# Performance work log

Hardware: AMD Instinct MI355X
Metric: run time of the kernel (lower is better)

Reference implementation:

```python
import jax, jax.numpy as jnp
import numpy as np

COST_CLS, COST_MASK, COST_DICE = 2.0, 5.0, 5.0


def setup_inputs() -> dict:
    key = jax.random.key(0)
    k1, k2, k3, k4 = jax.random.split(key, 4)
    B, Q, C, H, W, T, Hg, Wg = 4, 100, 81, 256, 256, 20, 512, 512
    pred_logits = jax.random.normal(k1, (B, Q, C), dtype=jnp.float32)
    pred_masks = jax.random.normal(k2, (B, Q, H, W), dtype=jnp.float32)
    # binary GT instance masks (original uses 0/1 masks)
    tgt_masks = (jax.random.uniform(k3, (B, T, Hg, Wg)) < 0.5).astype(jnp.float32)
    tgt_labels = jax.random.randint(k4, (B, T), 0, C).astype(jnp.int64)
    return {"pred_logits": pred_logits, "pred_masks": pred_masks,
            "tgt_masks": tgt_masks, "tgt_labels": tgt_labels}


def _cost_matrices(pred_logits, pred_masks, tgt_masks, tgt_labels):
    # pred_logits [B,Q,C], pred_masks [B,Q,H,W], tgt_masks [B,T,Hg,Wg], tgt_labels [B,T]
    B, Q, H, W = pred_masks.shape
    T, Hg, Wg = tgt_masks.shape[1:]
    # F.interpolate(mode='nearest') down to pred mask size: src = floor(dst * in/out)
    ri = (jnp.arange(H) * Hg) // H
    ci = (jnp.arange(W) * Wg) // W
    tgt = tgt_masks[:, :, ri][:, :, :, ci]          # [B,T,H,W]
    pm = pred_masks.reshape(B, Q, H * W)            # [B,Q,HW]
    tm = tgt.reshape(B, T, H * W)                   # [B,T,HW]
    hw = float(H * W)
    # classification cost: -softmax(logits)[:, tgt_ids]
    prob = jax.nn.softmax(pred_logits, axis=-1)     # [B,Q,C]
    cost_class = -jnp.take_along_axis(prob, tgt_labels[:, None, :], axis=2)  # [B,Q,T]
    # batch_sigmoid_ce_loss: mean over pixels of BCE-with-logits vs 0/1 target
    pos = jax.nn.softplus(-pm)                      # -log sigmoid(x)
    neg = jax.nn.softplus(pm)                       # -log (1 - sigmoid(x))
    cost_mask = (jnp.einsum('bqp,btp->bqt', pos, tm)
                 + jnp.einsum('bqp,btp->bqt', neg, 1.0 - tm)) / hw
    # batch_dice_loss
    sig = jax.nn.sigmoid(pm)
    numer = 2.0 * jnp.einsum('bqp,btp->bqt', sig, tm)
    denom = sig.sum(-1)[:, :, None] + tm.sum(-1)[:, None, :]
    cost_dice = 1.0 - (numer + 1.0) / (denom + 1.0)
    C = COST_CLS * cost_class + COST_MASK * cost_mask + COST_DICE * cost_dice
    return jnp.nan_to_num(C, nan=0.0)               # [B,Q,T]


_cost_jit = jax.jit(_cost_matrices)


def _lsa(cost):
    """Shortest-augmenting-path linear sum assignment (scipy algorithm).
    cost: (R, Cn) numpy array with R <= Cn. Returns col4row[r] = assigned column."""
    R, Cn = cost.shape
    u = np.zeros(R, dtype=np.float64)
    v = np.zeros(Cn, dtype=np.float64)
    col4row = np.full(R, -1, dtype=np.int64)
    row4col = np.full(Cn, -1, dtype=np.int64)
    cost = cost.astype(np.float64)
    for cur_row in range(R):
        shortest = np.full(Cn, np.inf)
        path = np.full(Cn, -1, dtype=np.int64)
        SR = np.zeros(R, dtype=bool)
        SC = np.zeros(Cn, dtype=bool)
        i = cur_row
        minVal = 0.0
        sink = -1
        while sink == -1:
            SR[i] = True
            rem = np.where(~SC)[0]
            d = minVal + cost[i, rem] - u[i] - v[rem]
            upd = d < shortest[rem]
            shortest[rem[upd]] = d[upd]
            path[rem[upd]] = i
            jloc = rem[np.argmin(shortest[rem])]
            minVal = shortest[jloc]
            SC[jloc] = True
            if row4col[jloc] == -1:
                sink = jloc
            else:
                i = row4col[jloc]
        u[cur_row] += minVal
        mask = SR.copy(); mask[cur_row] = False
        u[mask] += minVal - shortest[col4row[mask]]
        v[SC] -= minVal - shortest[SC]
        j = sink
        while True:
            i = path[j]
            row4col[j] = i
            col4row[i], j = j, col4row[i]
            if i == cur_row:
                break
    return col4row


def reference(pred_logits, pred_masks, tgt_masks, tgt_labels):
    C = _cost_jit(pred_logits, pred_masks, tgt_masks, tgt_labels)  # [B,Q,T]
    Cn = np.asarray(C)
    B, Q, T = Cn.shape
    pred_idx, tgt_idx = [], []
    for b in range(B):
        # solve on the transpose (T <= Q): target t -> query q[t]
        q = _lsa(Cn[b].T)
        t = np.arange(T)
        order = np.argsort(q)  # scipy returns row (query) indices in sorted order
        pred_idx.append(q[order])
        tgt_idx.append(t[order])
    return (C,
            jnp.asarray(np.stack(pred_idx), dtype=jnp.int64),
            jnp.asarray(np.stack(tgt_idx), dtype=jnp.int64))
```

## Files before the change

kernel.cpp:

```cpp
#include <hip/hip_runtime.h>
#include <hip/hip_bf16.h>
#include <math.h>
#include <stdint.h>

#define NB 4
#define NQ 100
#define NQR 101
#define NCLS 81
#define NT 20
#define NHW 65536

#define SC 256
#define CPX (NHW / SC)
#define TP 32

typedef __attribute__((ext_vector_type(8))) short bf16x8;
typedef __attribute__((ext_vector_type(16))) float f32x16;

__device__ inline short to_bf16(float f) {
    __hip_bfloat16 h = __float2bfloat16(f);
    return __builtin_bit_cast(short, h);
}

__device__ inline float fast_exp2(float x) { return __builtin_amdgcn_exp2f(x); }
__device__ inline float fast_log2(float x) { return __builtin_amdgcn_logf(x); }

__global__ void __launch_bounds__(256)
k_main(const float* __restrict__ pm, const float* __restrict__ tgt,
       float* __restrict__ A_part, float* __restrict__ D_part,
       float* __restrict__ Sp_part) {
    int gid = blockIdx.x;
    int chunk = gid & (SC - 1);
    int b = gid >> 8;
    int tid = threadIdx.x;
    int wv = tid >> 6, lane = tid & 63;
    int p0 = chunk * CPX;

    __shared__ uint32_t s_tb[CPX];
    __shared__ float s_pm[128 * 64];
    __shared__ short s_bf[4][512];

    if (tid < 128) {
        const float* base = tgt + (((size_t)b * NT) * 512 + 2 * chunk) * 512 + 4 * tid;
        uint32_t w0 = 0, w1 = 0;
#pragma unroll
        for (int t = 0; t < NT; ++t) {
            float4 v = *reinterpret_cast<const float4*>(base + (size_t)t * 512 * 512);
            w0 |= (v.x > 0.5f ? 1u : 0u) << t;
            w1 |= (v.z > 0.5f ? 1u : 0u) << t;
        }
        s_tb[2 * tid] = w0;
        s_tb[2 * tid + 1] = w1;
    }
    __syncthreads();

    int r0 = tid >> 4, cw = tid & 15;
    int Rg = wv * 32 + (lane & 31);
    int h = lane >> 5;
    const bool ones_row = (Rg == NQ);
    bf16x8 ones;
#pragma unroll
    for (int e = 0; e < 8; ++e) ones[e] = (short)0x3F80;

    f32x16 accA, accD;
#pragma unroll
    for (int r = 0; r < 16; ++r) { accA[r] = 0.0f; accD[r] = 0.0f; }
    float mxsum = 0.0f, l2sum = 0.0f;
    const float LOG2E = 1.4426950408889634f;

    for (int st = 0; st < 4; ++st) {
        {
            int ls = wv;
            int col = lane & 31;
            int kbase = st * 64 + ls * 16 + (h << 3);
            uint32_t pk[4];
#pragma unroll
            for (int e2 = 0; e2 < 4; ++e2) {
                uint32_t w0 = s_tb[kbase + 2 * e2];
                uint32_t w1 = s_tb[kbase + 2 * e2 + 1];
                uint32_t lo, hi;
                if (col < NT)       { lo = ((w0 >> col) & 1u) ? 0x3F80u : 0u;
                                      hi = ((w1 >> col) & 1u) ? 0x3F80u : 0u; }
                else if (col == NT) { lo = 0x3F80u; hi = 0x3F80u; }
                else                { lo = 0u; hi = 0u; }
                pk[e2] = lo | (hi << 16);
            }
            *reinterpret_cast<uint4*>(&s_bf[ls][lane * 8]) =
                *reinterpret_cast<const uint4*>(pk);
        }
#pragma unroll
        for (int p = 0; p < 8; ++p) {
            int row = r0 + 16 * p;
            int srow = (row < NQ) ? row : 0;
            float4 v = *reinterpret_cast<const float4*>(
                pm + ((size_t)(b * NQ + srow)) * NHW + (p0 + st * 64 + cw * 4));
            *reinterpret_cast<float4*>(
                &s_pm[row * 64 + ((cw ^ (row & 7)) << 2)]) = v;
        }
        __syncthreads();
#pragma unroll
        for (int sl = 0; sl < 4; ++sl) {
            int c0 = sl * 4 + h * 2;
            float4 xa = *reinterpret_cast<const float4*>(
                &s_pm[Rg * 64 + ((c0 ^ (Rg & 7)) << 2)]);
            float4 xb4 = *reinterpret_cast<const float4*>(
                &s_pm[Rg * 64 + (((c0 + 1) ^ (Rg & 7)) << 2)]);
            float xs[8] = {xa.x, xa.y, xa.z, xa.w, xb4.x, xb4.y, xb4.z, xb4.w};
            bf16x8 af, sf;
#pragma unroll
            for (int e = 0; e < 8; ++e) {
                float xi = xs[e];
                float y = xi * LOG2E;
                float e1 = fast_exp2(0.0f - fabsf(y));
                float tt = 1.0f + e1;
                float inv = __builtin_amdgcn_rcpf(tt);
                float sig = (xi >= 0.0f) ? inv : e1 * inv;
                l2sum += fast_log2(tt);
                mxsum += fmaxf(xi, 0.0f);
                af[e] = to_bf16(xi);
                sf[e] = to_bf16(sig);
            }
            if (ones_row) af = ones;
            bf16x8 bf = *reinterpret_cast<const bf16x8*>(&s_bf[sl][lane * 8]);
            accA = __builtin_amdgcn_mfma_f32_32x32x16_bf16(af, bf, accA, 0, 0, 0);
            accD = __builtin_amdgcn_mfma_f32_32x32x16_bf16(sf, bf, accD, 0, 0, 0);
        }
        __syncthreads();
    }

    int t = lane & 31;
#pragma unroll
    for (int r = 0; r < 16; ++r) {
        int rowD = (r & 3) + 8 * (r >> 2) + 4 * (lane >> 5);
        int qo = wv * 32 + rowD;
        if (qo <= NQ && t <= NT) {
            size_t base = ((size_t)(b * NQR + qo) * SC + chunk) * TP + t;
            A_part[base] = accA[r];
            D_part[base] = accD[r];
        }
    }
    float sp = fmaf(0.6931471805599453f, l2sum, mxsum);
    sp += __shfl_xor(sp, 32);
    if (lane < 32 && Rg < NQ)
        Sp_part[(size_t)(b * NQ + Rg) * SC + chunk] = sp;
}

__global__ void __launch_bounds__(256)
k_assemble(const float* __restrict__ logits, const int* __restrict__ labels,
           const float* __restrict__ A_part, const float* __restrict__ D_part,
           const float* __restrict__ Sp_part, float* __restrict__ Cout) {
    int bq = blockIdx.x;
    int q = bq % NQ, b = bq / NQ;
    int tid = threadIdx.x, wv = tid >> 6, lane = tid & 63;
    int t = tid & 31, g = tid >> 5;
    __shared__ float sA[4][32], sD[4][32], sS[4][32], sSn[4];

    const float* pa = A_part + (size_t)(b * NQR + q) * SC * TP;
    const float* pd = D_part + (size_t)(b * NQR + q) * SC * TP;
    const float* ps = A_part + (size_t)(b * NQR + NQ) * SC * TP;
    const float* pp = Sp_part + (size_t)(b * NQ + q) * SC;

    float a = 0.0f, d = 0.0f, s = 0.0f;
    for (int c = g; c < SC; c += 8) {
        a += pa[c * TP + t];
        d += pd[c * TP + t];
        s += ps[c * TP + t];
    }
    a += __shfl_xor(a, 32);
    d += __shfl_xor(d, 32);
    s += __shfl_xor(s, 32);
    if (lane < 32) { sA[wv][lane] = a; sD[wv][lane] = d; sS[wv][lane] = s; }
    {
        float sp = pp[tid];
        for (int o = 32; o; o >>= 1) sp += __shfl_xor(sp, o);
        if (lane == 0) sSn[wv] = sp;
    }
    __syncthreads();

    if (wv == 0) {
        int lt = (lane < 32) ? lane : 0;
        float At4 = sA[0][lt] + sA[1][lt] + sA[2][lt] + sA[3][lt];
        float Dt4 = sD[0][lt] + sD[1][lt] + sD[2][lt] + sD[3][lt];
        float St4 = sS[0][lt] + sS[1][lt] + sS[2][lt] + sS[3][lt];
        float Sneg = sSn[0] + sSn[1] + sSn[2] + sSn[3];
        float Ssig = __shfl(Dt4, NT);

        const float* lg = logits + (size_t)bq * NCLS;
        float x0 = (lane < NCLS) ? lg[lane] : -INFINITY;
        float x1 = (lane + 64 < NCLS) ? lg[lane + 64] : -INFINITY;
        float mx = fmaxf(x0, x1);
        for (int o = 32; o; o >>= 1) mx = fmaxf(mx, __shfl_xor(mx, o));
        float s0 = (lane < NCLS) ? __expf(x0 - mx) : 0.0f;
        float s1 = (lane + 64 < NCLS) ? __expf(x1 - mx) : 0.0f;
        float sum = s0 + s1;
        for (int o = 32; o; o >>= 1) sum += __shfl_xor(sum, o);

        if (lane < NT) {
            int label = labels[b * NT + lane];
            float prob = __expf(lg[label] - mx) / sum;
            float cm = (Sneg - At4) * (1.0f / (float)NHW);
            float cd = 1.0f - (2.0f * Dt4 + 1.0f) / (Ssig + St4 + 1.0f);
            float c = 2.0f * (-prob) + 5.0f * cm + 5.0f * cd;
            if (isnan(c)) c = 0.0f;
            Cout[(size_t)bq * NT + lane] = c;
        }
    }
}

__global__ void __launch_bounds__(64)
k_lsa(const float* __restrict__ Cmat, float* __restrict__ out) {
    int b = blockIdx.x;
    int lane = threadIdx.x;
    __shared__ double s_cost[NT][128];

    for (int idx = lane; idx < NT * 128; idx += 64) {
        int r = idx >> 7, j = idx & 127;
        s_cost[r][j] = (j < NQ) ? (double)Cmat[((size_t)b * NQ + j) * NT + r] : 0.0;
    }
    __syncthreads();

    int j0 = lane, j1 = lane + 64;
    bool v1ok = (j1 < NQ);
    double v_0 = 0.0, v_1 = 0.0;
    int r4c0 = -1, r4c1 = -1;
    double u_r = 0.0;
    int c4r = -1;

    for (int cur = 0; cur < NT; ++cur) {
        double sh0 = INFINITY, sh1 = INFINITY;
        int p0 = -1, p1 = -1;
        bool sc0 = false, sc1 = false;
        bool SRr = false;
        int i = cur, sink = -1;
        double minVal = 0.0;

        while (true) {
            if (lane == i) SRr = true;
            double ui = __shfl(u_r, i);
            double c0 = s_cost[i][j0];
            double c1 = s_cost[i][j1 & 127];
            if (!sc0) {
                double d = (minVal + c0 - ui) - v_0;
                if (d < sh0) { sh0 = d; p0 = i; }
            }
            if (v1ok && !sc1) {
                double d = (minVal + c1 - ui) - v_1;
                if (d < sh1) { sh1 = d; p1 = i; }
            }
            double cand0 = (!sc0) ? sh0 : INFINITY;
            double cand1 = (v1ok && !sc1) ? sh1 : INFINITY;
            double bv; int bj;
            if (cand0 <= cand1) { bv = cand0; bj = j0; }
            else                { bv = cand1; bj = j1; }
            for (int o = 32; o; o >>= 1) {
                double ov = __shfl_xor(bv, o);
                int oj = __shfl_xor(bj, o);
                if (ov < bv || (ov == bv && oj < bj)) { bv = ov; bj = oj; }
            }
            minVal = bv;
            if (bj < 64) { if (lane == bj) sc0 = true; }
            else         { if (lane == bj - 64) sc1 = true; }
            int r4 = (bj < 64) ? __shfl(r4c0, bj) : __shfl(r4c1, bj - 64);
            if (r4 == -1) { sink = bj; break; }
            i = r4;
        }

        {
            int c = c4r;
            double g0 = __shfl(sh0, c & 63);
            double g1 = __shfl(sh1, (c - 64) & 63);
            double shc = (c < 64) ? g0 : g1;
            if (lane == cur) u_r += minVal;
            else if (lane < NT && SRr) u_r += minVal - shc;
        }
        if (sc0) v_0 -= minVal - sh0;
        if (v1ok && sc1) v_1 -= minVal - sh1;

        int j = sink;
        while (true) {
            int ii = (j < 64) ? __shfl(p0, j) : __shfl(p1, j - 64);
            if (j < 64) { if (lane == j) r4c0 = ii; }
            else        { if (lane == j - 64) r4c1 = ii; }
            int nj = __shfl(c4r, ii);
            if (lane == ii) c4r = j;
            if (ii == cur) break;
            j = nj;
        }
    }

    int my = c4r;
    int rank = 0;
#pragma unroll
    for (int t2 = 0; t2 < NT; ++t2) {
        int vv = __shfl(my, t2);
        rank += (vv < my) ? 1 : 0;
    }
    if (lane < NT) {
        out[NB * NQ * NT + b * NT + rank] = (float)my;
        out[NB * NQ * NT + NB * NT + b * NT + rank] = (float)lane;
    }
}

extern "C" void kernel_launch(void* const* d_in, const int* in_sizes, int n_in,
                              void* d_out, int out_size, void* d_ws, size_t ws_size,
                              hipStream_t stream) {
    const float* pred_logits = (const float*)d_in[0];
    const float* pred_masks  = (const float*)d_in[1];
    const float* tgt_masks   = (const float*)d_in[2];
    const int*   tgt_labels  = (const int*)d_in[3];
    float* out = (float*)d_out;

    char* ws = (char*)d_ws;
    float* A_part  = (float*)ws;
    float* D_part  = A_part + (size_t)NB * NQR * SC * TP;
    float* Sp_part = D_part + (size_t)NB * NQR * SC * TP;

    k_main<<<NB * SC, 256, 0, stream>>>(pred_masks, tgt_masks, A_part, D_part, Sp_part);
    k_assemble<<<NB * NQ, 256, 0, stream>>>(pred_logits, tgt_labels, A_part, D_part,
                                            Sp_part, out);
    k_lsa<<<NB, 64, 0, stream>>>(out, out);
}
```

Before: 79.68 us.

## Stage pred masks as bf16 in LDS with larger 128-pixel stages

Pred mask values are now converted to bf16 while being loaded from global memory and stored packed in shared memory. Each stage covers 128 pixels instead of 64, so the loop runs 2 stages instead of 4. Loading only the 100 real rows with a 16-way XOR swizzle is meant to halve LDS footprint and traffic and cut barrier count. The trade-off is that the softplus and sigmoid terms are now computed from bf16-rounded inputs, which lowers the precision of the mask cost statistics.

```diff
diff --git a/kernel.cpp b/kernel.cpp
--- a/kernel.cpp
+++ b/kernel.cpp
@@ -20,6 +20,9 @@
 __device__ inline short to_bf16(float f) {
     __hip_bfloat16 h = __float2bfloat16(f);
     return __builtin_bit_cast(short, h);
+}
+__device__ inline float from_bf16(short s) {
+    return __builtin_bit_cast(float, ((uint32_t)(uint16_t)s) << 16);
 }
 
 __device__ inline float fast_exp2(float x) { return __builtin_amdgcn_exp2f(x); }
@@ -37,8 +40,8 @@
     int p0 = chunk * CPX;
 
     __shared__ uint32_t s_tb[CPX];
-    __shared__ float s_pm[128 * 64];
-    __shared__ short s_bf[4][512];
+    __shared__ short s_pm[100 * 128];
+    __shared__ short s_bf[8][512];
 
     if (tid < 128) {
         const float* base = tgt + (((size_t)b * NT) * 512 + 2 * chunk) * 512 + 4 * tid;
@@ -54,8 +57,8 @@
     }
     __syncthreads();
 
-    int r0 = tid >> 4, cw = tid & 15;
     int Rg = wv * 32 + (lane & 31);
+    int rcl = (Rg < NQ) ? Rg : 0;
     int h = lane >> 5;
     const bool ones_row = (Rg == NQ);
     bf16x8 ones;
@@ -68,11 +71,11 @@
     float mxsum = 0.0f, l2sum = 0.0f;
     const float LOG2E = 1.4426950408889634f;
 
-    for (int st = 0; st < 4; ++st) {
-        {
-            int ls = wv;
-            int col = lane & 31;
-            int kbase = st * 64 + ls * 16 + (h << 3);
+    for (int st = 0; st < 2; ++st) {
+        for (int e0 = tid; e0 < 512; e0 += 256) {
+            int ks = e0 >> 6, l = e0 & 63;
+            int col = l & 31;
+            int kbase = st * 128 + ks * 16 + ((l >> 5) << 3);
             uint32_t pk[4];
 #pragma unroll
             for (int e2 = 0; e2 < 4; ++e2) {
@@ -85,31 +88,37 @@
                 else                { lo = 0u; hi = 0u; }
                 pk[e2] = lo | (hi << 16);
             }
-            *reinterpret_cast<uint4*>(&s_bf[ls][lane * 8]) =
+            *reinterpret_cast<uint4*>(&s_bf[ks][l * 8]) =
                 *reinterpret_cast<const uint4*>(pk);
         }
-#pragma unroll
-        for (int p = 0; p < 8; ++p) {
-            int row = r0 + 16 * p;
-            int srow = (row < NQ) ? row : 0;
-            float4 v = *reinterpret_cast<const float4*>(
-                pm + ((size_t)(b * NQ + srow)) * NHW + (p0 + st * 64 + cw * 4));
-            *reinterpret_cast<float4*>(
-                &s_pm[row * 64 + ((cw ^ (row & 7)) << 2)]) = v;
+        for (int ch = tid; ch < 1600; ch += 256) {
+            int row = ch >> 4, cw = ch & 15;
+            int sw = cw ^ (row & 15);
+            const float* g = pm + ((size_t)(b * NQ + row)) * NHW
+                                + (p0 + st * 128 + sw * 8);
+            float4 f0 = *reinterpret_cast<const float4*>(g);
+            float4 f1 = *reinterpret_cast<const float4*>(g + 4);
+            uint32_t q0 = (uint32_t)(uint16_t)to_bf16(f0.x)
+                        | ((uint32_t)(uint16_t)to_bf16(f0.y) << 16);
+            uint32_t q1 = (uint32_t)(uint16_t)to_bf16(f0.z)
+                        | ((uint32_t)(uint16_t)to_bf16(f0.w) << 16);
+            uint32_t q2 = (uint32_t)(uint16_t)to_bf16(f1.x)
+                        | ((uint32_t)(uint16_t)to_bf16(f1.y) << 16);
+            uint32_t q3 = (uint32_t)(uint16_t)to_bf16(f1.z)
+                        | ((uint32_t)(uint16_t)to_bf16(f1.w) << 16);
+            uint4 pkw = make_uint4(q0, q1, q2, q3);
+            *reinterpret_cast<uint4*>(&s_pm[row * 128 + cw * 8]) = pkw;
         }
         __syncthreads();
 #pragma unroll
-        for (int sl = 0; sl < 4; ++sl) {
-            int c0 = sl * 4 + h * 2;
-            float4 xa = *reinterpret_cast<const float4*>(
-                &s_pm[Rg * 64 + ((c0 ^ (Rg & 7)) << 2)]);
-            float4 xb4 = *reinterpret_cast<const float4*>(
-                &s_pm[Rg * 64 + (((c0 + 1) ^ (Rg & 7)) << 2)]);
-            float xs[8] = {xa.x, xa.y, xa.z, xa.w, xb4.x, xb4.y, xb4.z, xb4.w};
-            bf16x8 af, sf;
+        for (int ks = 0; ks < 8; ++ks) {
+            int c = ks * 2 + h;
+            bf16x8 af = *reinterpret_cast<const bf16x8*>(
+                &s_pm[rcl * 128 + ((c ^ (rcl & 15)) << 3)]);
+            bf16x8 sf;
 #pragma unroll
             for (int e = 0; e < 8; ++e) {
-                float xi = xs[e];
+                float xi = from_bf16(af[e]);
                 float y = xi * LOG2E;
                 float e1 = fast_exp2(0.0f - fabsf(y));
                 float tt = 1.0f + e1;
@@ -117,13 +126,12 @@
                 float sig = (xi >= 0.0f) ? inv : e1 * inv;
                 l2sum += fast_log2(tt);
                 mxsum += fmaxf(xi, 0.0f);
-                af[e] = to_bf16(xi);
                 sf[e] = to_bf16(sig);
             }
             if (ones_row) af = ones;
-            bf16x8 bf = *reinterpret_cast<const bf16x8*>(&s_bf[sl][lane * 8]);
-            accA = __builtin_amdgcn_mfma_f32_32x32x16_bf16(af, bf, accA, 0, 0, 0);
-            accD = __builtin_amdgcn_mfma_f32_32x32x16_bf16(sf, bf, accD, 0, 0, 0);
+            bf16x8 bfv = *reinterpret_cast<const bf16x8*>(&s_bf[ks][lane * 8]);
+            accA = __builtin_amdgcn_mfma_f32_32x32x16_bf16(af, bfv, accA, 0, 0, 0);
+            accD = __builtin_amdgcn_mfma_f32_32x32x16_bf16(sf, bfv, accD, 0, 0, 0);
         }
         __syncthreads();
     }
```

After: 83.62 us. 1.05x slower.

## Load pred masks directly into registers and halve chunk count with precomputed target tiles

Applied to the files above, without the earlier changes.

Halves the number of pixel chunks per batch so each block covers 512 pixels, and precomputes all bf16 target-mask fragments into shared memory once at the start. The staged shared-memory copy of pred masks and the per-stage barriers are removed; each lane now reads its 8 pixel values straight from global memory as float4 loads. This cuts shared-memory traffic and synchronisation and halves the partial-sum volume that the assemble kernel must reduce. In exchange, global loads become strided per query row with less coalescing, and the grid has fewer blocks.

```diff
diff --git a/kernel.cpp b/kernel.cpp
--- a/kernel.cpp
+++ b/kernel.cpp
@@ -10,8 +10,9 @@
 #define NT 20
 #define NHW 65536
 
-#define SC 256
+#define SC 128
 #define CPX (NHW / SC)
+#define KST (CPX / 16)
 #define TP 32
 
 typedef __attribute__((ext_vector_type(8))) short bf16x8;
@@ -31,17 +32,18 @@
        float* __restrict__ Sp_part) {
     int gid = blockIdx.x;
     int chunk = gid & (SC - 1);
-    int b = gid >> 8;
+    int b = gid >> 7;
     int tid = threadIdx.x;
     int wv = tid >> 6, lane = tid & 63;
     int p0 = chunk * CPX;
 
     __shared__ uint32_t s_tb[CPX];
-    __shared__ float s_pm[128 * 64];
-    __shared__ short s_bf[4][512];
-
-    if (tid < 128) {
-        const float* base = tgt + (((size_t)b * NT) * 512 + 2 * chunk) * 512 + 4 * tid;
+    __shared__ short s_bf[KST][512];
+
+    {
+        int hrow = 2 * (p0 >> 8) + 2 * (tid >> 7);
+        int c4 = 4 * (tid & 127);
+        const float* base = tgt + (((size_t)b * NT) * 512 + hrow) * 512 + c4;
         uint32_t w0 = 0, w1 = 0;
 #pragma unroll
         for (int t = 0; t < NT; ++t) {
@@ -54,13 +56,34 @@
     }
     __syncthreads();
 
-    int r0 = tid >> 4, cw = tid & 15;
-    int Rg = wv * 32 + (lane & 31);
-    int h = lane >> 5;
-    const bool ones_row = (Rg == NQ);
+    for (int c = tid; c < KST * 64; c += 256) {
+        int ls = c >> 6, l = c & 63;
+        int col = l & 31;
+        int kbase = ls * 16 + ((l >> 5) << 3);
+        uint32_t pk[4];
+#pragma unroll
+        for (int e2 = 0; e2 < 4; ++e2) {
+            uint32_t w0 = s_tb[kbase + 2 * e2];
+            uint32_t w1 = s_tb[kbase + 2 * e2 + 1];
+            uint32_t lo, hi;
+            if (col < NT)       { lo = ((w0 >> col) & 1u) ? 0x3F80u : 0u;
+                                  hi = ((w1 >> col) & 1u) ? 0x3F80u : 0u; }
+            else if (col == NT) { lo = 0x3F80u; hi = 0x3F80u; }
+            else                { lo = 0u; hi = 0u; }
+            pk[e2] = lo | (hi << 16);
+        }
+        *reinterpret_cast<uint4*>(&s_bf[ls][l * 8]) = *reinterpret_cast<const uint4*>(pk);
+    }
+    __syncthreads();
+
+    int q = wv * 32 + (lane & 31);
+    int qc = (q < NQ) ? q : 0;
+    const bool ones_row = (q == NQ);
     bf16x8 ones;
 #pragma unroll
     for (int e = 0; e < 8; ++e) ones[e] = (short)0x3F80;
+    const float4* xp = reinterpret_cast<const float4*>(
+        pm + ((size_t)(b * NQ + qc)) * NHW + p0 + ((lane >> 5) << 3));
 
     f32x16 accA, accD;
 #pragma unroll
@@ -68,64 +91,29 @@
     float mxsum = 0.0f, l2sum = 0.0f;
     const float LOG2E = 1.4426950408889634f;
 
-    for (int st = 0; st < 4; ++st) {
-        {
-            int ls = wv;
-            int col = lane & 31;
-            int kbase = st * 64 + ls * 16 + (h << 3);
-            uint32_t pk[4];
-#pragma unroll
-            for (int e2 = 0; e2 < 4; ++e2) {
-                uint32_t w0 = s_tb[kbase + 2 * e2];
-                uint32_t w1 = s_tb[kbase + 2 * e2 + 1];
-                uint32_t lo, hi;
-                if (col < NT)       { lo = ((w0 >> col) & 1u) ? 0x3F80u : 0u;
-                                      hi = ((w1 >> col) & 1u) ? 0x3F80u : 0u; }
-                else if (col == NT) { lo = 0x3F80u; hi = 0x3F80u; }
-                else                { lo = 0u; hi = 0u; }
-                pk[e2] = lo | (hi << 16);
-            }
-            *reinterpret_cast<uint4*>(&s_bf[ls][lane * 8]) =
-                *reinterpret_cast<const uint4*>(pk);
-        }
-#pragma unroll
-        for (int p = 0; p < 8; ++p) {
-            int row = r0 + 16 * p;
-            int srow = (row < NQ) ? row : 0;
-            float4 v = *reinterpret_cast<const float4*>(
-                pm + ((size_t)(b * NQ + srow)) * NHW + (p0 + st * 64 + cw * 4));
-            *reinterpret_cast<float4*>(
-                &s_pm[row * 64 + ((cw ^ (row & 7)) << 2)]) = v;
-        }
-        __syncthreads();
-#pragma unroll
-        for (int sl = 0; sl < 4; ++sl) {
-            int c0 = sl * 4 + h * 2;
-            float4 xa = *reinterpret_cast<const float4*>(
-                &s_pm[Rg * 64 + ((c0 ^ (Rg & 7)) << 2)]);
-            float4 xb4 = *reinterpret_cast<const float4*>(
-                &s_pm[Rg * 64 + (((c0 + 1) ^ (Rg & 7)) << 2)]);
-            float xs[8] = {xa.x, xa.y, xa.z, xa.w, xb4.x, xb4.y, xb4.z, xb4.w};
-            bf16x8 af, sf;
-#pragma unroll
-            for (int e = 0; e < 8; ++e) {
-                float xi = xs[e];
-                float y = xi * LOG2E;
-                float e1 = fast_exp2(0.0f - fabsf(y));
-                float tt = 1.0f + e1;
-                float inv = __builtin_amdgcn_rcpf(tt);
-                float sig = (xi >= 0.0f) ? inv : e1 * inv;
-                l2sum += fast_log2(tt);
-                mxsum += fmaxf(xi, 0.0f);
-                af[e] = to_bf16(xi);
-                sf[e] = to_bf16(sig);
-            }
-            if (ones_row) af = ones;
-            bf16x8 bf = *reinterpret_cast<const bf16x8*>(&s_bf[sl][lane * 8]);
-            accA = __builtin_amdgcn_mfma_f32_32x32x16_bf16(af, bf, accA, 0, 0, 0);
-            accD = __builtin_amdgcn_mfma_f32_32x32x16_bf16(sf, bf, accD, 0, 0, 0);
-        }
-        __syncthreads();
+#pragma unroll 4
+    for (int s = 0; s < KST; ++s) {
+        float4 xa = xp[s * 4];
+        float4 xb4 = xp[s * 4 + 1];
+        float xs[8] = {xa.x, xa.y, xa.z, xa.w, xb4.x, xb4.y, xb4.z, xb4.w};
+        bf16x8 af, sf;
+#pragma unroll
+        for (int e = 0; e < 8; ++e) {
+            float xi = xs[e];
+            float y = xi * LOG2E;
+            float e1 = fast_exp2(0.0f - fabsf(y));
+            float tt = 1.0f + e1;
+            float inv = __builtin_amdgcn_rcpf(tt);
+            float sig = (xi >= 0.0f) ? inv : e1 * inv;
+            l2sum += fast_log2(tt);
+            mxsum += fmaxf(xi, 0.0f);
+            af[e] = to_bf16(xi);
+            sf[e] = to_bf16(sig);
+        }
+        if (ones_row) af = ones;
+        bf16x8 bf = *reinterpret_cast<const bf16x8*>(&s_bf[s][lane * 8]);
+        accA = __builtin_amdgcn_mfma_f32_32x32x16_bf16(af, bf, accA, 0, 0, 0);
+        accD = __builtin_amdgcn_mfma_f32_32x32x16_bf16(sf, bf, accD, 0, 0, 0);
     }
 
     int t = lane & 31;
@@ -141,8 +129,8 @@
     }
     float sp = fmaf(0.6931471805599453f, l2sum, mxsum);
     sp += __shfl_xor(sp, 32);
-    if (lane < 32 && Rg < NQ)
-        Sp_part[(size_t)(b * NQ + Rg) * SC + chunk] = sp;
+    if (lane < 32 && q < NQ)
+        Sp_part[(size_t)(b * NQ + q) * SC + chunk] = sp;
 }
 
 __global__ void __launch_bounds__(256)
@@ -171,7 +159,7 @@
     s += __shfl_xor(s, 32);
     if (lane < 32) { sA[wv][lane] = a; sD[wv][lane] = d; sS[wv][lane] = s; }
     {
-        float sp = pp[tid];
+        float sp = (tid < SC) ? pp[tid] : 0.0f;
         for (int o = 32; o; o >>= 1) sp += __shfl_xor(sp, o);
         if (lane == 0) sSn[wv] = sp;
     }
```

After: 80.30 us. No clear change (+0.8%).
